# Performance work log

Measured on AMD Instinct MI355X. Metric: run time of the kernel, lower is better.

Reference implementation:

```python
import jax, jax.numpy as jnp
import numpy as np
from jax import lax

C, H, W = 256, 56, 56
KP, STRIDE = 9, 2
M_CH, D, T = 64, 128, 16
TOPK = 32
SIGMA, ALPHA, TAU, EPS = 3.0, 10.0, 10.0, 1e-6
B = 4
N = H * W
PAD = KP // 2


def _build_M_P(h, w, s):
    ys = np.arange(0, h, s)
    xs = np.arange(0, w, s)
    ny, nx = len(ys), len(xs)
    N_, K_ = h * w, ny * nx
    by, bx = np.meshgrid(np.arange(h, dtype=np.float32), np.arange(w, dtype=np.float32), indexing='ij')
    bx = bx.reshape(-1)
    by = by.reshape(-1)
    fx, fy = bx / float(s), by / float(s)
    x0 = np.floor(fx).astype(np.int64)
    y0 = np.floor(fy).astype(np.int64)
    x0c = np.clip(x0, 0, nx - 1)
    x1c = np.clip(x0 + 1, 0, nx - 1)
    y0c = np.clip(y0, 0, ny - 1)
    y1c = np.clip(y0 + 1, 0, ny - 1)
    wx = fx - x0
    wy = fy - y0
    Mm = np.zeros((N_, K_), dtype=np.float32)
    rows = np.arange(N_)
    Mm[rows, y0c * nx + x0c] += (1 - wx) * (1 - wy)
    Mm[rows, y0c * nx + x1c] += wx * (1 - wy)
    Mm[rows, y1c * nx + x0c] += (1 - wx) * wy
    Mm[rows, y1c * nx + x1c] += wx * wy
    rs = Mm.sum(1, keepdims=True)
    rs[rs == 0] = 1.0
    Mm = Mm / rs
    P = np.stack([bx, by], axis=-1).astype(np.float32)  # (N,2) (x,y)
    return Mm, P


def _forward(feature_map, A_bank, pw_w, pw_b, proj_w, proj_b, r, M, P):
    def make_grid(A):  # affine_grid, align_corners=False
        xs = (2.0 * jnp.arange(W, dtype=jnp.float32) + 1.0) / W - 1.0
        ys = (2.0 * jnp.arange(H, dtype=jnp.float32) + 1.0) / H - 1.0
        gy, gx = jnp.meshgrid(ys, xs, indexing='ij')
        base = jnp.stack([gx, gy, jnp.ones_like(gx)], axis=-1)  # (H,W,3)
        return base @ A.T  # (H,W,2) normalized (x,y)

    def grid_sample(grid):  # bilinear, border padding, align_corners=False
        ix = ((grid[..., 0] + 1.0) * W - 1.0) / 2.0
        iy = ((grid[..., 1] + 1.0) * H - 1.0) / 2.0
        x0 = jnp.floor(ix)
        y0 = jnp.floor(iy)
        wx = ix - x0
        wy = iy - y0
        x0c = jnp.clip(x0, 0, W - 1).astype(jnp.int32)
        x1c = jnp.clip(x0 + 1, 0, W - 1).astype(jnp.int32)
        y0c = jnp.clip(y0, 0, H - 1).astype(jnp.int32)
        y1c = jnp.clip(y0 + 1, 0, H - 1).astype(jnp.int32)
        fm = feature_map.reshape(B, C, H * W)
        def g(yc, xc):
            return fm[:, :, (yc * W + xc).reshape(-1)].reshape(B, C, H, W)
        return (g(y0c, x0c) * (1 - wx) * (1 - wy) + g(y0c, x1c) * wx * (1 - wy)
                + g(y1c, x0c) * (1 - wx) * wy + g(y1c, x1c) * wx * wy)

    grids = jax.vmap(make_grid)(A_bank)          # (T,H,W,2)
    warped = jax.vmap(grid_sample)(grids)        # (T,B,C,H,W)

    # unfold(k,pad,stride) -> 1x1 conv -> spatial mean  ==  zero-padded avg-pool then linear
    pm = lax.reduce_window(warped, 0.0, lax.add,
                           (1, 1, 1, KP, KP), (1, 1, 1, STRIDE, STRIDE),
                           [(0, 0), (0, 0), (0, 0), (PAD, PAD), (PAD, PAD)]) / (KP * KP)
    Tn, Bn, Cn, Kh, Kw = pm.shape
    K = Kh * Kw
    pm = pm.reshape(Tn, Bn, Cn, K).transpose(0, 1, 3, 2)  # (T,B,K,C)
    x = pm @ pw_w.T + pw_b                                 # (T,B,K,m)
    z = x @ proj_w.T + proj_b                              # (T,B,K,d)
    z = z / jnp.maximum(jnp.linalg.norm(z, axis=-1, keepdims=True), EPS)
    Z = z.transpose(1, 0, 2, 3)                            # (B,T,K,d)

    s = jnp.einsum('btkd,d->btk', Z, r)
    wgt = jax.nn.softmax(TAU * s, axis=1)[..., None]
    g_emb = jnp.sum(wgt * Z, axis=1)                       # (B,K,d)

    E = jnp.einsum('nk,bkd->bnd', M, g_emb)
    E = E / jnp.maximum(jnp.linalg.norm(E, axis=-1, keepdims=True), EPS)

    d2 = jnp.sum((P[:, None, :] - P[None, :, :]) ** 2, axis=-1)  # (N,N)
    G = 1.0 - jnp.exp(-d2 / (2.0 * SIGMA ** 2))
    Saff = jnp.einsum('bnd,bmd->bnm', E, E) * G

    vals, idx = lax.top_k(Saff, TOPK)
    bidx = jnp.arange(B)[:, None, None]
    nidx = jnp.arange(N)[None, :, None]
    S_sp = jnp.zeros_like(Saff).at[bidx, nidx, idx].set(vals)
    A0 = jax.nn.softmax(ALPHA * S_sp, axis=-1) * jax.nn.softmax(ALPHA * S_sp, axis=-2)
    return E, A0


def setup_inputs() -> dict:
    key = jax.random.key(0)
    ks = jax.random.split(key, 6)
    feature_map = jax.random.normal(ks[0], (B, C, H, W), jnp.float32)
    ident = jnp.broadcast_to(jnp.array([[1.0, 0.0, 0.0], [0.0, 1.0, 0.0]], jnp.float32), (T, 2, 3))
    A_bank = ident + 0.1 * jax.random.normal(ks[1], (T, 2, 3), jnp.float32)
    pw_w = jax.random.normal(ks[2], (M_CH, C), jnp.float32) / np.sqrt(C).astype(np.float32)
    pw_b = jnp.zeros((M_CH,), jnp.float32)
    proj_w = jax.random.normal(ks[3], (D, M_CH), jnp.float32) / np.sqrt(M_CH).astype(np.float32)
    proj_b = jnp.zeros((D,), jnp.float32)
    r = 0.01 * jax.random.normal(ks[4], (D,), jnp.float32)
    Mnp, Pnp = _build_M_P(H, W, STRIDE)
    return {'feature_map': feature_map, 'A_bank': A_bank, 'pw_w': pw_w, 'pw_b': pw_b,
            'proj_w': proj_w, 'proj_b': proj_b, 'r': r,
            'M': jnp.asarray(Mnp), 'P': jnp.asarray(Pnp)}


def reference(feature_map, A_bank, pw_w, pw_b, proj_w, proj_b, r, M, P):
    return _forward(feature_map, A_bank, pw_w, pw_b, proj_w, proj_b, r, M, P)
```

## Files before the change

kernel.cpp:

```cpp
#include <hip/hip_runtime.h>
#include <hip/hip_bf16.h>
#include <hip/hip_fp16.h>

#define Hh 56
#define Ww 56
#define Cc 256
#define Tt 16
#define Bb 4
#define Nn 3136
#define Kk 784
#define KX 28
#define Dd 128
#define Mc 64
#define NTOP 32

typedef __attribute__((ext_vector_type(8))) _Float16 f16x8;
typedef __attribute__((ext_vector_type(4))) float f32x4;

__global__ __launch_bounds__(128) void k_wc(
    const float* __restrict__ pw_w, const float* __restrict__ pw_b,
    const float* __restrict__ proj_w, const float* __restrict__ proj_b,
    float* __restrict__ wct, float* __restrict__ bc) {
  int c = blockIdx.x;
  int d = threadIdx.x;
  float acc = 0.f;
  for (int m = 0; m < Mc; ++m) acc += proj_w[d * Mc + m] * pw_w[m * Cc + c];
  wct[c * Dd + d] = acc;
  if (c == 0) {
    float bb = proj_b[d];
    for (int m = 0; m < Mc; ++m) bb += proj_w[d * Mc + m] * pw_b[m];
    bc[d] = bb;
  }
}

__global__ __launch_bounds__(256) void k_coords(
    const float* __restrict__ Abank, unsigned* __restrict__ offo,
    float2* __restrict__ wo) {
  int t = blockIdx.x;
  const float* A = Abank + t * 6;
  float a00 = A[0], a01 = A[1], a02 = A[2], a10 = A[3], a11 = A[4], a12 = A[5];
  for (int e = threadIdx.x; e < Nn; e += 256) {
    int h = e / 56, w = e - h * 56;
    float gx = (2.0f * w + 1.0f) / 56.0f - 1.0f;
    float gy = (2.0f * h + 1.0f) / 56.0f - 1.0f;
    float u = a00 * gx + a01 * gy + a02;
    float v = a10 * gx + a11 * gy + a12;
    float ix = ((u + 1.0f) * 56.0f - 1.0f) * 0.5f;
    float iy = ((v + 1.0f) * 56.0f - 1.0f) * 0.5f;
    float x0f = floorf(ix), y0f = floorf(iy);
    int x0 = (int)x0f, y0 = (int)y0f;
    int x0c = min(max(x0, 0), 55), x1c = min(max(x0 + 1, 0), 55);
    int y0c = min(max(y0, 0), 55), y1c = min(max(y0 + 1, 0), 55);
    offo[t * Nn + e] = (y0c * 56 + x0c) | ((x1c - x0c) << 12) | ((y1c - y0c) << 13);
    float2 wv2;
    wv2.x = ix - x0f;
    wv2.y = iy - y0f;
    wo[t * Nn + e] = wv2;
  }
}

__global__ __launch_bounds__(256) void k_mix(
    const float* __restrict__ fm, const float* __restrict__ wct, float* __restrict__ y) {
  int blk = blockIdx.x;
  int b = blk / 98;
  int n0 = (blk % 98) * 32;
  int tid = threadIdx.x;
  int d = tid & 127;
  int ng = tid >> 7;
  __shared__ __align__(16) float fm_s[64][32];
  __shared__ float wc_s[64 * Dd];
  float acc[16];
#pragma unroll
  for (int j = 0; j < 16; ++j) acc[j] = 0.f;
  const float* fb = fm + (size_t)b * Cc * Nn;
  for (int c0 = 0; c0 < Cc; c0 += 64) {
    for (int i = tid; i < 64 * 32; i += 256) {
      int c = i >> 5, kx = i & 31;
      fm_s[c][kx] = fb[(size_t)(c0 + c) * Nn + n0 + kx];
    }
    for (int i = tid; i < 64 * Dd; i += 256) wc_s[i] = wct[c0 * Dd + i];
    __syncthreads();
    for (int c = 0; c < 64; ++c) {
      float w = wc_s[c * Dd + d];
      const float4* fr = reinterpret_cast<const float4*>(&fm_s[c][ng * 16]);
      float4 f0 = fr[0], f1 = fr[1], f2 = fr[2], f3 = fr[3];
      acc[0]  += f0.x * w; acc[1]  += f0.y * w; acc[2]  += f0.z * w; acc[3]  += f0.w * w;
      acc[4]  += f1.x * w; acc[5]  += f1.y * w; acc[6]  += f1.z * w; acc[7]  += f1.w * w;
      acc[8]  += f2.x * w; acc[9]  += f2.y * w; acc[10] += f2.z * w; acc[11] += f2.w * w;
      acc[12] += f3.x * w; acc[13] += f3.y * w; acc[14] += f3.z * w; acc[15] += f3.w * w;
    }
    __syncthreads();
  }
  size_t base = (((size_t)b * 64 + (d >> 1)) * Nn + n0 + ng * 16) * 2 + (d & 1);
#pragma unroll
  for (int j = 0; j < 16; ++j) y[base + 2 * j] = acc[j];
}

__global__ __launch_bounds__(256) void k_fused_pool(
    const float* __restrict__ yraw, const unsigned* __restrict__ offo,
    const float2* __restrict__ wo, const float* __restrict__ bc,
    float* __restrict__ zt) {
  const float2* y2 = reinterpret_cast<const float2*>(yraw);
  int idx = blockIdx.x;
  int b = idx & 3;
  int pg = (idx >> 2) & 31;
  int t = idx >> 7;
  __shared__ float2 wsm[3136];
  __shared__ float2 rowp[1568];
  int tid = threadIdx.x;
  const unsigned* offp = offo + t * Nn;
  const float2* wp = wo + t * Nn;
  unsigned off[13];
  float2 wv[13];
#pragma unroll
  for (int j = 0; j < 13; ++j) {
    int e = tid + 256 * j;
    if (e < 3136) {
      off[j] = offp[e];
      wv[j] = wp[e];
    }
  }
  for (int pp = 0; pp < 2; ++pp) {
    int dp = pg * 2 + pp;
    const float2* fc = y2 + ((size_t)b * 64 + dp) * Nn;
    float b0 = bc[dp * 2], b1 = bc[dp * 2 + 1];
#pragma unroll
    for (int j = 0; j < 13; ++j) {
      int e = tid + 256 * j;
      if (e < 3136) {
        unsigned pk = off[j];
        int base = pk & 4095;
        int dx = (pk >> 12) & 1;
        int dyy = (pk & (1u << 13)) ? 56 : 0;
        float2 v00 = fc[base], v01 = fc[base + dx];
        float2 v10 = fc[base + dyy], v11 = fc[base + dyy + dx];
        float wx = wv[j].x, wy = wv[j].y;
        float tx = v00.x + wx * (v01.x - v00.x);
        float bx = v10.x + wx * (v11.x - v10.x);
        float ty = v00.y + wx * (v01.y - v00.y);
        float by = v10.y + wx * (v11.y - v10.y);
        float2 o;
        o.x = tx + wy * (bx - tx);
        o.y = ty + wy * (by - ty);
        wsm[e] = o;
      }
    }
    __syncthreads();
    for (int e = tid; e < 1568; e += 256) {
      int h = e / 28, kx = e - h * 28;
      int xs = 2 * kx - 4;
      int lo = max(xs, 0), hi = min(xs + 8, 55);
      float sx = 0.f, sy = 0.f;
      const float2* wr = wsm + h * 56;
      for (int x = lo; x <= hi; ++x) { float2 v = wr[x]; sx += v.x; sy += v.y; }
      float2 o; o.x = sx; o.y = sy;
      rowp[e] = o;
    }
    __syncthreads();
    float* zo0 = zt + ((size_t)(t * Bb + b) * Dd + dp * 2) * Kk;
    float* zo1 = zo0 + Kk;
    for (int e = tid; e < 784; e += 256) {
      int ky = e / 28, kx = e - ky * 28;
      int ys = 2 * ky - 4;
      int lo = max(ys, 0), hi = min(ys + 8, 55);
      float sx = 0.f, sy = 0.f;
      for (int h = lo; h <= hi; ++h) { float2 rv = rowp[h * 28 + kx]; sx += rv.x; sy += rv.y; }
      zo0[e] = sx * (1.0f / 81.0f) + b0;
      zo1[e] = sy * (1.0f / 81.0f) + b1;
    }
    __syncthreads();
  }
}

__global__ __launch_bounds__(256) void k_znorm(
    const float* __restrict__ zt, const float* __restrict__ r,
    float* __restrict__ z, float* __restrict__ s_arr) {
  int tb = blockIdx.x / 14;
  int k0 = (blockIdx.x % 14) * 56;
  int tid = threadIdx.x;
  __shared__ float ls[56 * 129];
  const float* zb = zt + (size_t)tb * Dd * Kk + k0;
  for (int i = tid; i < Dd * 56; i += 256) {
    int d = i / 56, kk = i - d * 56;
    ls[kk * 129 + d] = zb[(size_t)d * Kk + kk];
  }
  int lane = tid & 63;
  int wvv = tid >> 6;
  float r0 = r[lane], r1 = r[lane + 64];
  __syncthreads();
  for (int p = 0; p < 14; ++p) {
    int k = p * 4 + wvv;
    float z0 = ls[k * 129 + lane];
    float z1 = ls[k * 129 + 64 + lane];
    float ss = z0 * z0 + z1 * z1;
    for (int off = 32; off; off >>= 1) ss += __shfl_xor(ss, off);
    float inv = 1.0f / fmaxf(sqrtf(ss), 1e-6f);
    z0 *= inv; z1 *= inv;
    float* zr = z + ((size_t)tb * Kk + k0 + k) * Dd;
    zr[lane] = z0;
    zr[lane + 64] = z1;
    float sd = z0 * r0 + z1 * r1;
    for (int off = 32; off; off >>= 1) sd += __shfl_xor(sd, off);
    if (lane == 0) s_arr[(size_t)tb * Kk + k0 + k] = sd;
  }
}

__global__ __launch_bounds__(128) void k_gemb(
    const float* __restrict__ z, const float* __restrict__ s_arr, float* __restrict__ g) {
  int blk = blockIdx.x;
  int b = blk / Kk, k = blk % Kk;
  int d = threadIdx.x;
  float sv[Tt];
  float mx = -3.4e38f;
#pragma unroll
  for (int t = 0; t < Tt; ++t) {
    sv[t] = s_arr[(t * Bb + b) * Kk + k];
    mx = fmaxf(mx, sv[t]);
  }
  float sum = 0.f;
#pragma unroll
  for (int t = 0; t < Tt; ++t) {
    sv[t] = expf(10.0f * (sv[t] - mx));
    sum += sv[t];
  }
  float isum = 1.0f / sum;
  float acc = 0.f;
#pragma unroll
  for (int t = 0; t < Tt; ++t)
    acc += sv[t] * isum * z[((size_t)(t * Bb + b) * Kk + k) * Dd + d];
  g[((size_t)b * Kk + k) * Dd + d] = acc;
}

__global__ __launch_bounds__(128) void k_E(
    const float* __restrict__ Mmat, const float* __restrict__ g,
    float* __restrict__ E, _Float16* __restrict__ E16) {
  int row = blockIdx.x * 2 + (threadIdx.x >> 6);
  int b = row / Nn, n = row % Nn;
  int y = n / Ww, x = n % Ww;
  int x0 = x >> 1, y0 = y >> 1;
  int x1 = min(x0 + 1, 27), y1 = min(y0 + 1, 27);
  bool hx = (x1 != x0), hy = (y1 != y0);
  int k00 = y0 * 28 + x0, k01 = y0 * 28 + x1, k10 = y1 * 28 + x0, k11 = y1 * 28 + x1;
  const float* Mr = Mmat + (size_t)n * Kk;
  float m00 = Mr[k00];
  float m01 = hx ? Mr[k01] : 0.f;
  float m10 = hy ? Mr[k10] : 0.f;
  float m11 = (hx && hy) ? Mr[k11] : 0.f;
  const float* gb = g + (size_t)b * Kk * Dd;
  int lane = threadIdx.x & 63;
  int l2 = lane + 64;
  float a0 = m00 * gb[k00 * Dd + lane] + m01 * gb[k01 * Dd + lane] +
             m10 * gb[k10 * Dd + lane] + m11 * gb[k11 * Dd + lane];
  float a1 = m00 * gb[k00 * Dd + l2] + m01 * gb[k01 * Dd + l2] +
             m10 * gb[k10 * Dd + l2] + m11 * gb[k11 * Dd + l2];
  float ss = a0 * a0 + a1 * a1;
  for (int off = 32; off; off >>= 1) ss += __shfl_xor(ss, off);
  float inv = 1.0f / fmaxf(sqrtf(ss), 1e-6f);
  float e0 = a0 * inv, e1 = a1 * inv;
  E[(size_t)row * Dd + lane] = e0;
  E[(size_t)row * Dd + l2] = e1;
  E16[(size_t)row * Dd + lane] = (_Float16)e0;
  E16[(size_t)row * Dd + l2] = (_Float16)e1;
}

__global__ __launch_bounds__(256) void k_saff(
    const _Float16* __restrict__ E16, __half* __restrict__ S) {
  int blk = blockIdx.x;
  int b = blk / 1225;
  int rem = blk % 1225;
  int ti0 = (int)((sqrtf(8.f * rem + 1.f) - 1.f) * 0.5f);
  while ((ti0 + 1) * (ti0 + 2) / 2 <= rem) ++ti0;
  while (ti0 * (ti0 + 1) / 2 > rem) --ti0;
  int tj0 = rem - ti0 * (ti0 + 1) / 2;
  int i0 = ti0 * 64, j0 = tj0 * 64;
  int wave = threadIdx.x >> 6, lane = threadIdx.x & 63;
  int wr = wave >> 1, wc = wave & 1;
  int lr = lane & 15, lk = lane >> 4;
  int ibase = i0 + wr * 32;
  int jbase = j0 + wc * 32;
  const _Float16* Eb = E16 + (size_t)b * Nn * Dd;
  __shared__ __half tile[64][66];
  f32x4 acc00 = {0.f, 0.f, 0.f, 0.f};
  f32x4 acc01 = acc00, acc10 = acc00, acc11 = acc00;
#pragma unroll
  for (int ks = 0; ks < 4; ++ks) {
    int ko = ks * 32 + lk * 8;
    f16x8 a0 = *reinterpret_cast<const f16x8*>(Eb + (size_t)(ibase + lr) * Dd + ko);
    f16x8 a1 = *reinterpret_cast<const f16x8*>(Eb + (size_t)(ibase + 16 + lr) * Dd + ko);
    f16x8 b0 = *reinterpret_cast<const f16x8*>(Eb + (size_t)(jbase + lr) * Dd + ko);
    f16x8 b1 = *reinterpret_cast<const f16x8*>(Eb + (size_t)(jbase + 16 + lr) * Dd + ko);
    acc00 = __builtin_amdgcn_mfma_f32_16x16x32_f16(a0, b0, acc00, 0, 0, 0);
    acc01 = __builtin_amdgcn_mfma_f32_16x16x32_f16(a0, b1, acc01, 0, 0, 0);
    acc10 = __builtin_amdgcn_mfma_f32_16x16x32_f16(a1, b0, acc10, 0, 0, 0);
    acc11 = __builtin_amdgcn_mfma_f32_16x16x32_f16(a1, b1, acc11, 0, 0, 0);
  }
  size_t ob = (size_t)b * Nn * Nn;
  int gj[2];
  float xj[2], yj[2];
#pragma unroll
  for (int tj = 0; tj < 2; ++tj) {
    gj[tj] = jbase + tj * 16 + lr;
    int yv = gj[tj] / 56;
    yj[tj] = (float)yv;
    xj[tj] = (float)(gj[tj] - yv * 56);
  }
  bool mirror = (i0 != j0);
#pragma unroll
  for (int ti = 0; ti < 2; ++ti) {
#pragma unroll
    for (int q = 0; q < 4; ++q) {
      int iloc = wr * 32 + ti * 16 + lk * 4 + q;
      int gi = i0 + iloc;
      int yiv = gi / 56;
      float yi = (float)yiv;
      float xi = (float)(gi - yiv * 56);
#pragma unroll
      for (int tj = 0; tj < 2; ++tj) {
        float a;
        if (ti == 0 && tj == 0) a = acc00[q];
        else if (ti == 0 && tj == 1) a = acc01[q];
        else if (ti == 1 && tj == 0) a = acc10[q];
        else a = acc11[q];
        float dx = xi - xj[tj];
        float dy = yi - yj[tj];
        float gg = 1.0f - __expf(-(dx * dx + dy * dy) * (1.0f / 18.0f));
        __half hv = __float2half(a * gg);
        S[ob + (size_t)gi * Nn + gj[tj]] = hv;
        int jloc = wc * 32 + tj * 16 + lr;
        tile[jloc][iloc] = hv;
      }
    }
  }
  if (mirror) {
    __syncthreads();
    for (int e = threadIdx.x; e < 64 * 32; e += 256) {
      int row = e >> 5, c2 = e & 31;
      unsigned v = *reinterpret_cast<const unsigned*>(&tile[row][c2 * 2]);
      *reinterpret_cast<unsigned*>(&S[ob + (size_t)(j0 + row) * Nn + i0 + c2 * 2]) = v;
    }
  }
}

__global__ __launch_bounds__(256) void k_topk(
    const __half* __restrict__ S16, const float* __restrict__ E,
    const float* __restrict__ P, float* __restrict__ topv, int* __restrict__ topi,
    float* __restrict__ dr, float* __restrict__ dc) {
  int row = blockIdx.x;
  int b = row / Nn, irow = row % Nn;
  int tid = threadIdx.x;
  const unsigned* Sr = reinterpret_cast<const unsigned*>(S16 + (size_t)row * Nn);
  __shared__ unsigned hist[256 * 8];
  __shared__ unsigned wtot[4];
  __shared__ unsigned bcast[2];
  __shared__ unsigned sel_eq, sel_slot;
  __shared__ int sel_idx[NTOP];
  __shared__ float drow_s;
  unsigned pk[7];
#pragma unroll
  for (int j = 0; j < 7; ++j) {
    int c2 = tid + 256 * j;
    unsigned u = (c2 < Nn / 2) ? Sr[c2] : 0u;
    unsigned h0 = u & 0xFFFFu, h1 = u >> 16;
    unsigned k0 = h0 ^ ((h0 & 0x8000u) ? 0xFFFFu : 0x8000u);
    unsigned k1 = h1 ^ ((h1 & 0x8000u) ? 0xFFFFu : 0x8000u);
    if (c2 >= Nn / 2) { k0 = 0u; k1 = 0u; }
    pk[j] = k0 | (k1 << 16);
  }
  if (tid == 0) { sel_eq = 0; sel_slot = 0; drow_s = 0.f; }
  int lane = tid & 63, wvq = tid >> 6;
  unsigned prefix = 0;
  unsigned k = NTOP;
  for (int pass = 0; pass < 2; ++pass) {
    int shift = 8 - 8 * pass;
    unsigned pmask = pass ? 0xFF00u : 0u;
#pragma unroll
    for (int i = 0; i < 8; ++i) hist[tid * 8 + i] = 0;
    __syncthreads();
#pragma unroll
    for (int j = 0; j < 7; ++j) {
      unsigned k0 = pk[j] & 0xFFFFu, k1 = pk[j] >> 16;
      if ((k0 & pmask) == (prefix & pmask))
        atomicAdd(&hist[((k0 >> shift) & 255u) * 8 + (tid & 7)], 1u);
      if ((k1 & pmask) == (prefix & pmask))
        atomicAdd(&hist[((k1 >> shift) & 255u) * 8 + (tid & 7)], 1u);
    }
    __syncthreads();
    unsigned cnt = 0;
#pragma unroll
    for (int i = 0; i < 8; ++i) cnt += hist[tid * 8 + i];
    unsigned run = cnt;
#pragma unroll
    for (int off2 = 1; off2 < 64; off2 <<= 1) {
      unsigned v = __shfl_down(run, off2);
      if (lane + off2 < 64) run += v;
    }
    if (lane == 0) wtot[wvq] = run;
    __syncthreads();
    unsigned hi = 0;
    for (int w2 = wvq + 1; w2 < 4; ++w2) hi += wtot[w2];
    unsigned incl = run + hi;
    unsigned excl = incl - cnt;
    if (excl < k && k <= incl) {
      bcast[0] = prefix | ((unsigned)tid << shift);
      bcast[1] = k - excl;
    }
    __syncthreads();
    prefix = bcast[0];
    k = bcast[1];
    __syncthreads();
  }
  unsigned T = prefix;
#pragma unroll
  for (int j = 0; j < 7; ++j) {
    int c2 = tid + 256 * j;
    if (c2 < Nn / 2) {
      unsigned k0 = pk[j] & 0xFFFFu, k1 = pk[j] >> 16;
      bool take0 = (k0 > T) || (k0 == T && atomicAdd(&sel_eq, 1u) < k);
      if (take0) { unsigned slot = atomicAdd(&sel_slot, 1u); sel_idx[slot] = 2 * c2; }
      bool take1 = (k1 > T) || (k1 == T && atomicAdd(&sel_eq, 1u) < k);
      if (take1) { unsigned slot = atomicAdd(&sel_slot, 1u); sel_idx[slot] = 2 * c2 + 1; }
    }
  }
  __syncthreads();
  int sel = tid >> 3, part = tid & 7;
  int col = sel_idx[sel];
  const float* Ei = E + ((size_t)b * Nn + irow) * Dd;
  const float* Ej = E + ((size_t)b * Nn + col) * Dd;
  float v = 0.f;
#pragma unroll
  for (int d0 = 0; d0 < 16; ++d0) {
    int d = part * 16 + d0;
    v += Ei[d] * Ej[d];
  }
  v += __shfl_xor(v, 1);
  v += __shfl_xor(v, 2);
  v += __shfl_xor(v, 4);
  if (part == 0) {
    float dx = P[irow * 2] - P[col * 2];
    float dy = P[irow * 2 + 1] - P[col * 2 + 1];
    float gg = 1.0f - __expf(-(dx * dx + dy * dy) * (1.0f / 18.0f));
    v *= gg;
    topv[(size_t)row * NTOP + sel] = v;
    topi[(size_t)row * NTOP + sel] = col;
    float e = __expf(10.f * v);
    atomicAdd(&dc[b * Nn + col], e - 1.f);
    atomicAdd(&drow_s, e);
  }
  __syncthreads();
  if (tid == 0) dr[row] = (float)(Nn - NTOP) + drow_s;
}

__global__ void k_dcinit(float* __restrict__ dc) {
  int i = blockIdx.x * 256 + threadIdx.x;
  if (i < Bb * Nn) dc[i] = (float)Nn;
}

__global__ void k_inv(float* __restrict__ dr, float* __restrict__ dc) {
  int i = blockIdx.x * 256 + threadIdx.x;
  if (i < Bb * Nn) {
    dr[i] = 1.0f / dr[i];
    dc[i] = 1.0f / dc[i];
  }
}

__global__ __launch_bounds__(256) void k_basefix(
    const float* __restrict__ invdr, const float* __restrict__ invdc,
    const float* __restrict__ topv, const int* __restrict__ topi,
    float* __restrict__ A0) {
  int row = blockIdx.x;
  int b = row / Nn;
  float idr = invdr[row];
  const float4* dc4 = reinterpret_cast<const float4*>(invdc + b * Nn);
  float4* out4 = reinterpret_cast<float4*>(A0 + (size_t)row * Nn);
  for (int j = threadIdx.x; j < Nn / 4; j += 256) {
    float4 c = dc4[j];
    float4 o = {idr * c.x, idr * c.y, idr * c.z, idr * c.w};
    out4[j] = o;
  }
  __syncthreads();
  if (threadIdx.x < NTOP) {
    int gidx = row * NTOP + threadIdx.x;
    int col = topi[gidx];
    float e = __expf(10.f * topv[gidx]);
    A0[(size_t)row * Nn + col] = e * e * idr * invdc[b * Nn + col];
  }
}

extern "C" void kernel_launch(void* const* d_in, const int* in_sizes, int n_in,
                              void* d_out, int out_size, void* d_ws, size_t ws_size,
                              hipStream_t stream) {
  const float* fm     = (const float*)d_in[0];
  const float* Abank  = (const float*)d_in[1];
  const float* pw_w   = (const float*)d_in[2];
  const float* pw_b   = (const float*)d_in[3];
  const float* proj_w = (const float*)d_in[4];
  const float* proj_b = (const float*)d_in[5];
  const float* r      = (const float*)d_in[6];
  const float* Mmat   = (const float*)d_in[7];
  const float* P      = (const float*)d_in[8];
  float* out = (float*)d_out;
  float* E  = out;
  float* A0 = out + (size_t)Bb * Nn * Dd;
  __half* S16 = (__half*)A0;

  float* ws = (float*)d_ws;
  float* y     = ws;
  float* zt    = ws + 1605632;
  float* z     = ws + 8028160;
  float* wct   = ws + 14450688;
  float* bcv   = ws + 14483456;
  float* s_arr = ws + 14483584;
  float* g     = ws + 14533760;
  float* topv  = ws + 14935168;
  int*   topi  = (int*)(ws + 15336576);
  float* dr    = ws + 15737984;
  float* dc    = ws + 15750528;
  _Float16* E16 = (_Float16*)(ws + 15763072);
  unsigned* offo = (unsigned*)(ws + 16565888);
  float2*   wo   = (float2*)(ws + 16616064);

  hipLaunchKernelGGL(k_wc, dim3(Cc), dim3(128), 0, stream, pw_w, pw_b, proj_w, proj_b, wct, bcv);
  hipLaunchKernelGGL(k_coords, dim3(Tt), dim3(256), 0, stream, Abank, offo, wo);
  hipLaunchKernelGGL(k_mix, dim3(392), dim3(256), 0, stream, fm, wct, y);
  hipLaunchKernelGGL(k_fused_pool, dim3(2048), dim3(256), 0, stream, y, offo, wo, bcv, zt);
  hipLaunchKernelGGL(k_znorm, dim3(64 * 14), dim3(256), 0, stream, zt, r, z, s_arr);
  hipLaunchKernelGGL(k_gemb, dim3(Bb * Kk), dim3(128), 0, stream, z, s_arr, g);
  hipLaunchKernelGGL(k_E, dim3(Bb * Nn / 2), dim3(128), 0, stream, Mmat, g, E, E16);
  hipLaunchKernelGGL(k_saff, dim3(Bb * 1225), dim3(256), 0, stream, E16, S16);
  hipLaunchKernelGGL(k_dcinit, dim3(49), dim3(256), 0, stream, dc);
  hipLaunchKernelGGL(k_topk, dim3(Bb * Nn), dim3(256), 0, stream, S16, E, P, topv, topi, dr, dc);
  hipLaunchKernelGGL(k_inv, dim3(49), dim3(256), 0, stream, dr, dc);
  hipLaunchKernelGGL(k_basefix, dim3(Bb * Nn), dim3(256), 0, stream, dr, dc, topv, topi, A0);
}
```

Baseline: 427.0 us.

## Merge prep kernels, widen pool channel batching, stage S writes through LDS

Three small prep kernels (weight compose, sampling coords, dc init) become one launch with block ranges dispatching to each job. The fused pool kernel now handles four channel pairs per block with half the grid, reusing the loaded offsets and weights more times. The affinity kernel stages the direct S tile in shared memory as well as the transposed one, then writes both out as coalesced 32-bit stores instead of scattered 16-bit stores. The costs are extra LDS, an unconditional barrier, and fewer pool blocks in flight.

```diff
diff --git a/kernel.cpp b/kernel.cpp
--- a/kernel.cpp
+++ b/kernel.cpp
@@ -17,45 +17,52 @@
 typedef __attribute__((ext_vector_type(8))) _Float16 f16x8;
 typedef __attribute__((ext_vector_type(4))) float f32x4;
 
-__global__ __launch_bounds__(128) void k_wc(
+__global__ __launch_bounds__(256) void k_prep(
     const float* __restrict__ pw_w, const float* __restrict__ pw_b,
     const float* __restrict__ proj_w, const float* __restrict__ proj_b,
-    float* __restrict__ wct, float* __restrict__ bc) {
-  int c = blockIdx.x;
-  int d = threadIdx.x;
-  float acc = 0.f;
-  for (int m = 0; m < Mc; ++m) acc += proj_w[d * Mc + m] * pw_w[m * Cc + c];
-  wct[c * Dd + d] = acc;
-  if (c == 0) {
-    float bb = proj_b[d];
-    for (int m = 0; m < Mc; ++m) bb += proj_w[d * Mc + m] * pw_b[m];
-    bc[d] = bb;
-  }
-}
-
-__global__ __launch_bounds__(256) void k_coords(
-    const float* __restrict__ Abank, unsigned* __restrict__ offo,
-    float2* __restrict__ wo) {
-  int t = blockIdx.x;
-  const float* A = Abank + t * 6;
-  float a00 = A[0], a01 = A[1], a02 = A[2], a10 = A[3], a11 = A[4], a12 = A[5];
-  for (int e = threadIdx.x; e < Nn; e += 256) {
-    int h = e / 56, w = e - h * 56;
-    float gx = (2.0f * w + 1.0f) / 56.0f - 1.0f;
-    float gy = (2.0f * h + 1.0f) / 56.0f - 1.0f;
-    float u = a00 * gx + a01 * gy + a02;
-    float v = a10 * gx + a11 * gy + a12;
-    float ix = ((u + 1.0f) * 56.0f - 1.0f) * 0.5f;
-    float iy = ((v + 1.0f) * 56.0f - 1.0f) * 0.5f;
-    float x0f = floorf(ix), y0f = floorf(iy);
-    int x0 = (int)x0f, y0 = (int)y0f;
-    int x0c = min(max(x0, 0), 55), x1c = min(max(x0 + 1, 0), 55);
-    int y0c = min(max(y0, 0), 55), y1c = min(max(y0 + 1, 0), 55);
-    offo[t * Nn + e] = (y0c * 56 + x0c) | ((x1c - x0c) << 12) | ((y1c - y0c) << 13);
-    float2 wv2;
-    wv2.x = ix - x0f;
-    wv2.y = iy - y0f;
-    wo[t * Nn + e] = wv2;
+    const float* __restrict__ Abank,
+    float* __restrict__ wct, float* __restrict__ bc,
+    unsigned* __restrict__ offo, float2* __restrict__ wo,
+    float* __restrict__ dc) {
+  int blk = blockIdx.x;
+  if (blk < 256) {
+    int c = blk;
+    int d = threadIdx.x;
+    if (d < 128) {
+      float acc = 0.f;
+      for (int m = 0; m < Mc; ++m) acc += proj_w[d * Mc + m] * pw_w[m * Cc + c];
+      wct[c * Dd + d] = acc;
+      if (c == 0) {
+        float bb = proj_b[d];
+        for (int m = 0; m < Mc; ++m) bb += proj_w[d * Mc + m] * pw_b[m];
+        bc[d] = bb;
+      }
+    }
+  } else if (blk < 272) {
+    int t = blk - 256;
+    const float* A = Abank + t * 6;
+    float a00 = A[0], a01 = A[1], a02 = A[2], a10 = A[3], a11 = A[4], a12 = A[5];
+    for (int e = threadIdx.x; e < Nn; e += 256) {
+      int h = e / 56, w = e - h * 56;
+      float gx = (2.0f * w + 1.0f) / 56.0f - 1.0f;
+      float gy = (2.0f * h + 1.0f) / 56.0f - 1.0f;
+      float u = a00 * gx + a01 * gy + a02;
+      float v = a10 * gx + a11 * gy + a12;
+      float ix = ((u + 1.0f) * 56.0f - 1.0f) * 0.5f;
+      float iy = ((v + 1.0f) * 56.0f - 1.0f) * 0.5f;
+      float x0f = floorf(ix), y0f = floorf(iy);
+      int x0 = (int)x0f, y0 = (int)y0f;
+      int x0c = min(max(x0, 0), 55), x1c = min(max(x0 + 1, 0), 55);
+      int y0c = min(max(y0, 0), 55), y1c = min(max(y0 + 1, 0), 55);
+      offo[t * Nn + e] = (y0c * 56 + x0c) | ((x1c - x0c) << 12) | ((y1c - y0c) << 13);
+      float2 wv2;
+      wv2.x = ix - x0f;
+      wv2.y = iy - y0f;
+      wo[t * Nn + e] = wv2;
+    }
+  } else {
+    int i = (blk - 272) * 256 + threadIdx.x;
+    if (i < Bb * Nn) dc[i] = (float)Nn;
   }
 }
 
@@ -103,8 +110,8 @@
   const float2* y2 = reinterpret_cast<const float2*>(yraw);
   int idx = blockIdx.x;
   int b = idx & 3;
-  int pg = (idx >> 2) & 31;
-  int t = idx >> 7;
+  int pg = (idx >> 2) & 15;
+  int t = idx >> 6;
   __shared__ float2 wsm[3136];
   __shared__ float2 rowp[1568];
   int tid = threadIdx.x;
@@ -120,8 +127,8 @@
       wv[j] = wp[e];
     }
   }
-  for (int pp = 0; pp < 2; ++pp) {
-    int dp = pg * 2 + pp;
+  for (int pp = 0; pp < 4; ++pp) {
+    int dp = pg * 4 + pp;
     const float2* fc = y2 + ((size_t)b * 64 + dp) * Nn;
     float b0 = bc[dp * 2], b1 = bc[dp * 2 + 1];
 #pragma unroll
@@ -279,7 +286,8 @@
   int ibase = i0 + wr * 32;
   int jbase = j0 + wc * 32;
   const _Float16* Eb = E16 + (size_t)b * Nn * Dd;
-  __shared__ __half tile[64][66];
+  __shared__ __half tileT[64][66];
+  __shared__ __half tileR[64][66];
   f32x4 acc00 = {0.f, 0.f, 0.f, 0.f};
   f32x4 acc01 = acc00, acc10 = acc00, acc11 = acc00;
 #pragma unroll
@@ -325,17 +333,22 @@
         float dy = yi - yj[tj];
         float gg = 1.0f - __expf(-(dx * dx + dy * dy) * (1.0f / 18.0f));
         __half hv = __float2half(a * gg);
-        S[ob + (size_t)gi * Nn + gj[tj]] = hv;
         int jloc = wc * 32 + tj * 16 + lr;
-        tile[jloc][iloc] = hv;
+        tileR[iloc][jloc] = hv;
+        tileT[jloc][iloc] = hv;
       }
     }
   }
+  __syncthreads();
+  for (int e = threadIdx.x; e < 64 * 32; e += 256) {
+    int row = e >> 5, c2 = e & 31;
+    unsigned v = *reinterpret_cast<const unsigned*>(&tileR[row][c2 * 2]);
+    *reinterpret_cast<unsigned*>(&S[ob + (size_t)(i0 + row) * Nn + j0 + c2 * 2]) = v;
+  }
   if (mirror) {
-    __syncthreads();
     for (int e = threadIdx.x; e < 64 * 32; e += 256) {
       int row = e >> 5, c2 = e & 31;
-      unsigned v = *reinterpret_cast<const unsigned*>(&tile[row][c2 * 2]);
+      unsigned v = *reinterpret_cast<const unsigned*>(&tileT[row][c2 * 2]);
       *reinterpret_cast<unsigned*>(&S[ob + (size_t)(j0 + row) * Nn + i0 + c2 * 2]) = v;
     }
   }
@@ -448,11 +461,6 @@
   }
   __syncthreads();
   if (tid == 0) dr[row] = (float)(Nn - NTOP) + drow_s;
-}
-
-__global__ void k_dcinit(float* __restrict__ dc) {
-  int i = blockIdx.x * 256 + threadIdx.x;
-  if (i < Bb * Nn) dc[i] = (float)Nn;
 }
 
 __global__ void k_inv(float* __restrict__ dr, float* __restrict__ dc) {
@@ -519,15 +527,14 @@
   unsigned* offo = (unsigned*)(ws + 16565888);
   float2*   wo   = (float2*)(ws + 16616064);
 
-  hipLaunchKernelGGL(k_wc, dim3(Cc), dim3(128), 0, stream, pw_w, pw_b, proj_w, proj_b, wct, bcv);
-  hipLaunchKernelGGL(k_coords, dim3(Tt), dim3(256), 0, stream, Abank, offo, wo);
+  hipLaunchKernelGGL(k_prep, dim3(321), dim3(256), 0, stream,
+                     pw_w, pw_b, proj_w, proj_b, Abank, wct, bcv, offo, wo, dc);
   hipLaunchKernelGGL(k_mix, dim3(392), dim3(256), 0, stream, fm, wct, y);
-  hipLaunchKernelGGL(k_fused_pool, dim3(2048), dim3(256), 0, stream, y, offo, wo, bcv, zt);
+  hipLaunchKernelGGL(k_fused_pool, dim3(1024), dim3(256), 0, stream, y, offo, wo, bcv, zt);
   hipLaunchKernelGGL(k_znorm, dim3(64 * 14), dim3(256), 0, stream, zt, r, z, s_arr);
   hipLaunchKernelGGL(k_gemb, dim3(Bb * Kk), dim3(128), 0, stream, z, s_arr, g);
   hipLaunchKernelGGL(k_E, dim3(Bb * Nn / 2), dim3(128), 0, stream, Mmat, g, E, E16);
   hipLaunchKernelGGL(k_saff, dim3(Bb * 1225), dim3(256), 0, stream, E16, S16);
-  hipLaunchKernelGGL(k_dcinit, dim3(49), dim3(256), 0, stream, dc);
   hipLaunchKernelGGL(k_topk, dim3(Bb * Nn), dim3(256), 0, stream, S16, E, P, topv, topi, dr, dc);
   hipLaunchKernelGGL(k_inv, dim3(49), dim3(256), 0, stream, dr, dc);
   hipLaunchKernelGGL(k_basefix, dim3(Bb * Nn), dim3(256), 0, stream, dr, dc, topv, topi, A0);
```

After: 434.0 us. Within noise of the previous version (+1.6%).
